# Kernel tuning notes

Hardware: AMD Instinct MI355X
Metric: run time of the kernel (lower is better)

The kernel has to match this reference:

```python
import jax, jax.numpy as jnp
import numpy as np

DIM = 2048
N_HEADS = 32
N_KV_HEADS = 8
HEAD_DIM = DIM // N_HEADS
ROPE_BASE = 10000.0
BATCH = 2
SEQ = 2048


def _rope_cos_sin(seq_len, dtype=jnp.float32):
    inv_freq = 1.0 / (ROPE_BASE ** (jnp.arange(0, HEAD_DIM, 2, dtype=jnp.float32) / HEAD_DIM))
    pos = jnp.arange(seq_len, dtype=jnp.float32)
    freqs = pos[:, None] * inv_freq[None, :]  # (seq, head_dim/2)
    return jnp.cos(freqs).astype(dtype), jnp.sin(freqs).astype(dtype)


def _apply_rope(x, cos, sin):
    # x: (b, h, s, d); cos/sin: (s, d/2). Interleaved (even/odd) RoPE.
    cos = cos[None, None, :, :]
    sin = sin[None, None, :, :]
    x_even = x[..., ::2]
    x_odd = x[..., 1::2]
    rot_even = x_even * cos - x_odd * sin
    rot_odd = x_even * sin + x_odd * cos
    out = jnp.stack((rot_even, rot_odd), axis=-1)
    return out.reshape(x.shape)


def setup_inputs() -> dict:
    key = jax.random.key(0)
    ks = jax.random.split(key, 5)
    s = 0.02
    return {
        "x": jax.random.normal(ks[0], (BATCH, SEQ, DIM), dtype=jnp.float32),
        "wq": jax.random.normal(ks[1], (DIM, N_HEADS * HEAD_DIM), dtype=jnp.float32) * s,
        "wk": jax.random.normal(ks[2], (DIM, N_KV_HEADS * HEAD_DIM), dtype=jnp.float32) * s,
        "wv": jax.random.normal(ks[3], (DIM, N_KV_HEADS * HEAD_DIM), dtype=jnp.float32) * s,
        "wo": jax.random.normal(ks[4], (DIM, DIM), dtype=jnp.float32) * s,
    }


def reference(x, wq, wk, wv, wo):
    b, s, _ = x.shape
    q = (x @ wq).reshape(b, s, N_HEADS, HEAD_DIM).transpose(0, 2, 1, 3)
    k = (x @ wk).reshape(b, s, N_KV_HEADS, HEAD_DIM).transpose(0, 2, 1, 3)
    v = (x @ wv).reshape(b, s, N_KV_HEADS, HEAD_DIM).transpose(0, 2, 1, 3)
    cos, sin = _rope_cos_sin(s, x.dtype)
    q = _apply_rope(q, cos, sin)
    k = _apply_rope(k, cos, sin)
    rep = N_HEADS // N_KV_HEADS
    if rep > 1:
        k = jnp.repeat(k, rep, axis=1)
        v = jnp.repeat(v, rep, axis=1)
    scores = jnp.einsum("bhqd,bhkd->bhqk", q, k) / (HEAD_DIM ** 0.5)
    causal = jnp.tril(jnp.ones((s, s), dtype=bool))
    scores = jnp.where(causal[None, None], scores, -jnp.inf)
    probs = jax.nn.softmax(scores, axis=-1)
    out = jnp.einsum("bhqk,bhkd->bhqd", probs, v)
    out = out.transpose(0, 2, 1, 3).reshape(b, s, DIM)
    return out @ wo
```

## Files before the change

### kernel.cpp

```cpp
#include <hip/hip_runtime.h>
#include <stdint.h>

#define DIM   2048
#define NH    32
#define NKV   8
#define HD    64
#define BATCH 2
#define SEQ   2048

typedef __attribute__((ext_vector_type(8))) short  short8;
typedef __attribute__((ext_vector_type(4))) short  short4v;
typedef __attribute__((ext_vector_type(4))) float  f32x4;

#if __has_builtin(__builtin_amdgcn_exp2f)
#define EXP2(x) __builtin_amdgcn_exp2f(x)
#else
#define EXP2(x) exp2f(x)
#endif

static __device__ __forceinline__ short f2bf(float f) {
  union { float f; uint32_t u; } v; v.f = f;
  uint32_t r = v.u + 0x7FFFu + ((v.u >> 16) & 1u);
  return (short)(r >> 16);
}

static __device__ __forceinline__ uint32_t cvtpk_bf16(float lo, float hi) {
  uint32_t r;
  asm("v_cvt_pk_bf16_f32 %0, %1, %2" : "=v"(r) : "v"(lo), "v"(hi));
  return r;
}

#define GLD16(gp, lp) __builtin_amdgcn_global_load_lds(                      \
    (__attribute__((address_space(1))) void*)(void*)(gp),                    \
    (__attribute__((address_space(3))) void*)(lp), 16, 0, 0)

#define QSCALE 0.1803368801111244f

__global__ void __launch_bounds__(256)
prep_kernel(const float* __restrict__ x, const float* __restrict__ wq,
            const float* __restrict__ wk, const float* __restrict__ wv,
            short* __restrict__ x_bf, short* __restrict__ wq_t,
            short* __restrict__ wk_t, short* __restrict__ wv_t,
            float* __restrict__ ct, float* __restrict__ st) {
  __shared__ float t[32][33];
  int blk = blockIdx.x;
  const int tid = threadIdx.x;
  if (blk < 8192) {
    int i = blk * 256 + tid;
    f32x4 v = *reinterpret_cast<const f32x4*>(x + (size_t)i * 4);
    short4v o;
    o.x = f2bf(v.x); o.y = f2bf(v.y); o.z = f2bf(v.z); o.w = f2bf(v.w);
    *reinterpret_cast<short4v*>(x_bf + (size_t)i * 4) = o;
    return;
  }
  blk -= 8192;
  if (blk < 6144) {
    const float* in; short* out; int C, bx, by;
    if (blk < 4096)      { in = wq; out = wq_t; C = 2048; bx = blk & 63; by = blk >> 6; }
    else if (blk < 5120) { int lo = blk - 4096; in = wk; out = wk_t; C = 512; bx = lo & 15; by = lo >> 4; }
    else                 { int lo = blk - 5120; in = wv; out = wv_t; C = 512; bx = lo & 15; by = lo >> 4; }
    const int c0 = bx * 32, r0 = by * 32;
    const int tx = tid & 31, ty = tid >> 5;
#pragma unroll
    for (int j = 0; j < 32; j += 8)
      t[ty + j][tx] = in[(size_t)(r0 + ty + j) * C + c0 + tx];
    __syncthreads();
#pragma unroll
    for (int j = 0; j < 32; j += 8)
      out[(size_t)(c0 + ty + j) * DIM + r0 + tx] = f2bf(t[tx][ty + j]);
    return;
  }
  blk -= 6144;
  {
    int i = blk * 256 + tid;
    int pos = i >> 5, f = i & 31;
    float inv = powf(10000.0f, -(float)f / 32.0f);
    float th = (float)pos * inv;
    ct[i] = cosf(th);
    st[i] = sinf(th);
  }
}

__global__ void transpose_bf_kernel(const float* __restrict__ in, short* __restrict__ out,
                                    int R, int C) {
  __shared__ float t[32][33];
  int c0 = blockIdx.x * 32, r0 = blockIdx.y * 32;
  int tx = threadIdx.x, ty = threadIdx.y;
#pragma unroll
  for (int j = 0; j < 32; j += 8)
    t[ty + j][tx] = in[(size_t)(r0 + ty + j) * C + c0 + tx];
  __syncthreads();
#pragma unroll
  for (int j = 0; j < 32; j += 8)
    out[(size_t)(c0 + ty + j) * R + r0 + tx] = f2bf(t[tx][ty + j]);
}


__device__ __forceinline__ void mfma_tile(const short* __restrict__ as_,
                                          const short* __restrict__ bs_,
                                          int wr, int wc, int lg, int lr,
                                          f32x4 (&acc)[4][4]) {
  short8 af[4], bq[4];
#pragma unroll
  for (int mt = 0; mt < 4; ++mt) {
    int row = wr * 64 + mt * 16 + lr;
    af[mt] = *(const short8*)&as_[row * 32 + ((lg ^ ((row >> 1) & 3)) << 3)];
  }
#pragma unroll
  for (int nt = 0; nt < 4; ++nt) {
    int row = wc * 64 + nt * 16 + lr;
    bq[nt] = *(const short8*)&bs_[row * 32 + ((lg ^ ((row >> 1) & 3)) << 3)];
  }
  __builtin_amdgcn_s_setprio(1);
#pragma unroll
  for (int mt = 0; mt < 4; ++mt)
#pragma unroll
    for (int nt = 0; nt < 4; ++nt)
      acc[mt][nt] = __builtin_amdgcn_mfma_f32_16x16x32_bf16(af[mt], bq[nt], acc[mt][nt], 0, 0, 0);
  __builtin_amdgcn_s_setprio(0);
}

#define STAGE4(SA, SB) do {                                                  \
    GLD16(pA0, (SA) + w * 512);  GLD16(pA1, (SA) + 2048 + w * 512);          \
    GLD16(pB0, (SB) + w * 512);  GLD16(pB1, (SB) + 2048 + w * 512);          \
    pA0 += 32; pA1 += 32; pB0 += 32; pB1 += 32; } while (0)

#define TILE(CA, CB, SA, SB, DOSTAGE, VM) do {                               \
    asm volatile("s_waitcnt vmcnt(" VM ")" ::: "memory");                    \
    __builtin_amdgcn_s_barrier();                                            \
    __builtin_amdgcn_sched_barrier(0);                                       \
    if (DOSTAGE) { STAGE4(SA, SB); }                                         \
    mfma_tile(CA, CB, wr, wc, lg, lr, acc);                                  \
  } while (0)

__device__ __forceinline__ void gemm_mainloop(const short* __restrict__ A,
                                              const short* __restrict__ Bt,
                                              int m0, int n0,
                                              short* As, short* Bs,
                                              f32x4 (&acc)[4][4]) {
  const int tid = threadIdx.x;
  const int w = tid >> 6, l = tid & 63;
  const int lg = l >> 4, lr = l & 15;
  const int wr = w >> 1, wc = w & 1;
  const int c1 = tid + 256;
  const int r0 = tid >> 2, k0 = ((tid & 3) ^ ((r0 >> 1) & 3)) << 3;
  const int r1 = c1 >> 2,  k1 = ((c1 & 3) ^ ((r1 >> 1) & 3)) << 3;
  const short* pA0 = A + (size_t)(m0 + r0) * DIM + k0;
  const short* pA1 = A + (size_t)(m0 + r1) * DIM + k1;
  const short* pB0 = Bt + (size_t)(n0 + r0) * DIM + k0;
  const short* pB1 = Bt + (size_t)(n0 + r1) * DIM + k1;
  short* A0 = As;            short* B0 = Bs;
  short* A1 = As + 4096;     short* B1 = Bs + 4096;
  short* A2 = As + 8192;     short* B2 = Bs + 8192;

  STAGE4(A0, B0);
  STAGE4(A1, B1);

  for (int it = 0; it < 20; ++it) {
    TILE(A0, B0, A2, B2, true, "4");
    TILE(A1, B1, A0, B0, true, "4");
    TILE(A2, B2, A1, B1, true, "4");
  }
  TILE(A0, B0, A2, B2, true,  "4");
  TILE(A1, B1, A0, B0, true,  "4");
  TILE(A2, B2, A0, B0, false, "4");
  TILE(A0, B0, A1, B1, false, "0");
}

__device__ __forceinline__ int2 xcd_swizzle(int nwg) {
  int id = blockIdx.y * gridDim.x + blockIdx.x;
  int swz = (id & 7) * (nwg >> 3) + (id >> 3);
  return make_int2(swz % gridDim.x, swz / gridDim.x);
}

__global__ void __launch_bounds__(256, 3)
gemm_qkv_kernel(const short* __restrict__ A,
                const short* __restrict__ wqt, const short* __restrict__ wkt,
                const short* __restrict__ wvt,
                short* __restrict__ q_ws, short* __restrict__ k_ws, short* __restrict__ v_ws,
                const float* __restrict__ ct, const float* __restrict__ st) {
  __shared__ __align__(16) short As[12288];
  __shared__ __align__(16) short Bs[12288];
  int2 bxy = xcd_swizzle(24 * 32);
  const int n0g = bxy.x * 128;
  const int m0 = bxy.y * 128;
  int mode, n0;
  const short* Bt;
  short* outp;
  if (n0g < 2048)      { mode = 1; Bt = wqt; n0 = n0g;        outp = q_ws; }
  else if (n0g < 2560) { mode = 2; Bt = wkt; n0 = n0g - 2048; outp = k_ws; }
  else                 { mode = 3; Bt = wvt; n0 = n0g - 2560; outp = v_ws; }

  f32x4 acc[4][4] = {};
  gemm_mainloop(A, Bt, m0, n0, As, Bs, acc);

  const int tid = threadIdx.x;
  const int w = tid >> 6, l = tid & 63;
  const int lg = l >> 4, lr = l & 15;
  const int wr = w >> 1, wc = w & 1;
  const int mrow0 = m0 + wr * 64;
  const int ncol0 = n0 + wc * 64;
#pragma unroll
  for (int mt = 0; mt < 4; ++mt)
#pragma unroll
    for (int nt = 0; nt < 4; ++nt)
#pragma unroll
      for (int i = 0; i < 4; ++i) {
        int m = mrow0 + mt * 16 + lg * 4 + i;
        int n = ncol0 + nt * 16 + lr;
        float v = acc[mt][nt][i];
        int b = m >> 11, s = m & (SEQ - 1);
        int h = n >> 6, d = n & 63;
        if (mode == 3) {
          outp[((size_t)(b * NKV + h) * HD + d) * SEQ + s] = f2bf(v);
        } else {
          float p = __shfl_xor(v, 1);
          float cs = ct[(s << 5) + (d >> 1)];
          float sn = st[(s << 5) + (d >> 1)];
          float r = ((d & 1) == 0) ? (v * cs - p * sn) : (p * sn + v * cs);
          if (mode == 1) {
            r *= QSCALE;
            outp[((size_t)(b * NH + h) * SEQ + s) * HD + d] = f2bf(r);
          } else {
            outp[((size_t)(b * NKV + h) * SEQ + s) * HD + d] = f2bf(r);
          }
        }
      }
}

__global__ void __launch_bounds__(256, 3)
gemm_o_kernel(const short* __restrict__ A, const short* __restrict__ Bt,
              float* __restrict__ out) {
  __shared__ __align__(16) short As[12288];
  __shared__ __align__(16) short Bs[12288];
  int2 bxy = xcd_swizzle(16 * 32);
  const int m0 = bxy.y * 128, n0 = bxy.x * 128;
  f32x4 acc[4][4] = {};
  gemm_mainloop(A, Bt, m0, n0, As, Bs, acc);
  const int tid = threadIdx.x;
  const int w = tid >> 6, l = tid & 63;
  const int lg = l >> 4, lr = l & 15;
  const int wr = w >> 1, wc = w & 1;
#pragma unroll
  for (int mt = 0; mt < 4; ++mt)
#pragma unroll
    for (int nt = 0; nt < 4; ++nt)
#pragma unroll
      for (int i = 0; i < 4; ++i) {
        int m = m0 + wr * 64 + mt * 16 + lg * 4 + i;
        int n = n0 + wc * 64 + nt * 16 + lr;
        out[(size_t)m * DIM + n] = acc[mt][nt][i];
      }
}

__global__ void __launch_bounds__(256, 3)
attn_fwd_kernel(const short* __restrict__ Q, const short* __restrict__ K,
                const short* __restrict__ V, short* __restrict__ O) {
  __shared__ __align__(16) short Ks[3][4096];
  __shared__ __align__(16) short Vs[3][4096];
  const int tid = threadIdx.x;
  const int w = tid >> 6, l = tid & 63;
  const int lg = l >> 4, lr = l & 15;
  const int h = blockIdx.y;
  const int b = blockIdx.z;
  const int kvh = h >> 2;
  const int lh = lg >> 1, sub = (lg & 1) << 2;

  const short* kbase = K + (size_t)(b * NKV + kvh) * SEQ * HD;
  const short* vbase = V + (size_t)(b * NKV + kvh) * HD * SEQ;

  const int c1 = tid + 256;
  const int r0 = tid >> 3, e0 = ((tid & 7) ^ (r0 & 7)) << 3;
  const int r1 = c1 >> 3, e1 = ((c1 & 7) ^ (r1 & 7)) << 3;

  short8 ones;
#pragma unroll
  for (int i = 0; i < 8; ++i) ones[i] = (short)0x3F80;

#define ASTAGE(kvt, KB, VB) do { const int kv_ = (kvt) * 64;                  \
    GLD16(kbase + (size_t)(kv_ + r0) * HD + e0, (KB) + w * 512);              \
    GLD16(kbase + (size_t)(kv_ + r1) * HD + e1, (KB) + 2048 + w * 512);       \
    GLD16(vbase + (size_t)r0 * SEQ + kv_ + e0, (VB) + w * 512);               \
    GLD16(vbase + (size_t)r1 * SEQ + kv_ + e1, (VB) + 2048 + w * 512); } while (0)

  for (int qi = 0; qi < 2; ++qi) {
    const int qblk = (qi == 0) ? (int)blockIdx.x : (31 - (int)blockIdx.x);
    const int q0 = qblk * 64;
    const int qrow = q0 + w * 16 + lr;

    const short* qptr = Q + ((size_t)(b * NH + h) * SEQ + qrow) * HD;
    short8 qf0 = *(const short8*)(qptr + (lg << 3));
    short8 qf1 = *(const short8*)(qptr + 32 + (lg << 3));

    float m_run = 0.f;
    f32x4 oacc[4] = {};
    f32x4 lacc = {};

    short* kb0 = Ks[0]; short* kb1 = Ks[1]; short* kb2 = Ks[2];
    short* vb0 = Vs[0]; short* vb1 = Vs[1]; short* vb2 = Vs[2];

    ASTAGE(0, kb0, vb0);
    if (qblk >= 1) ASTAGE(1, kb1, vb1);

    for (int t = 0; t <= qblk; ++t) {
      if (t < qblk) asm volatile("s_waitcnt vmcnt(4)" ::: "memory");
      else          asm volatile("s_waitcnt vmcnt(0)" ::: "memory");
      __builtin_amdgcn_s_barrier();
      __builtin_amdgcn_sched_barrier(0);
      if (t + 2 <= qblk) ASTAGE(t + 2, kb2, vb2);

      const short* ks = kb0;
      const short* vs = vb0;
      const int kv0 = t * 64;

      short8 ka[4][2];
#pragma unroll
      for (int t4 = 0; t4 < 4; ++t4) {
        int row = t4 * 16 + lr, rx = row & 7;
        ka[t4][0] = *(const short8*)&ks[row * 64 + ((lg ^ rx) << 3)];
        ka[t4][1] = *(const short8*)&ks[row * 64 + (((4 + lg) ^ rx) << 3)];
      }
      short8 vbf[4][2];
#pragma unroll
      for (int nt = 0; nt < 4; ++nt) {
        int row = nt * 16 + lr, rx = row & 7;
#pragma unroll
        for (int ks_ = 0; ks_ < 2; ++ks_) {
          union { short8 s8; short4v hh[2]; } u;
          u.hh[0] = *(const short4v*)&vs[row * 64 + (((4 * ks_ + lh) ^ rx) << 3) + sub];
          u.hh[1] = *(const short4v*)&vs[row * 64 + (((4 * ks_ + 2 + lh) ^ rx) << 3) + sub];
          vbf[nt][ks_] = u.s8;
        }
      }

      f32x4 sacc[4];
      {
        f32x4 seed;
        seed[0] = -m_run; seed[1] = -m_run; seed[2] = -m_run; seed[3] = -m_run;
        __builtin_amdgcn_s_setprio(1);
#pragma unroll
        for (int t4 = 0; t4 < 4; ++t4) {
          f32x4 z = __builtin_amdgcn_mfma_f32_16x16x32_bf16(ka[t4][0], qf0, seed, 0, 0, 0);
          sacc[t4] = __builtin_amdgcn_mfma_f32_16x16x32_bf16(ka[t4][1], qf1, z, 0, 0, 0);
        }
        __builtin_amdgcn_s_setprio(0);
      }

      if (t == qblk) {
#pragma unroll
        for (int t4 = 0; t4 < 4; ++t4)
#pragma unroll
          for (int i = 0; i < 4; ++i)
            if (kv0 + t4 * 16 + lg * 4 + i > qrow) sacc[t4][i] = -__builtin_inff();
      }

      float a0 = fmaxf(fmaxf(sacc[0][0], sacc[0][1]), sacc[0][2]);
      float a1 = fmaxf(fmaxf(sacc[0][3], sacc[1][0]), sacc[1][1]);
      float a2 = fmaxf(fmaxf(sacc[1][2], sacc[1][3]), sacc[2][0]);
      float a3 = fmaxf(fmaxf(sacc[2][1], sacc[2][2]), sacc[2][3]);
      float a4 = fmaxf(fmaxf(sacc[3][0], sacc[3][1]), sacc[3][2]);
      float tm = fmaxf(fmaxf(fmaxf(a0, a1), a2), fmaxf(fmaxf(a3, a4), sacc[3][3]));
      tm = fmaxf(tm, __shfl_xor(tm, 16));
      tm = fmaxf(tm, __shfl_xor(tm, 32));

      if (!__all(tm <= 12.0f)) {
        float d = fmaxf(tm, 0.f);
        float alpha = EXP2(-d);
        float av0 = __shfl(alpha, (lg << 2));
        float av1 = __shfl(alpha, (lg << 2) | 1);
        float av2 = __shfl(alpha, (lg << 2) | 2);
        float av3 = __shfl(alpha, (lg << 2) | 3);
#pragma unroll
        for (int nt = 0; nt < 4; ++nt) {
          oacc[nt][0] *= av0; oacc[nt][1] *= av1;
          oacc[nt][2] *= av2; oacc[nt][3] *= av3;
        }
        lacc[0] *= av0; lacc[1] *= av1; lacc[2] *= av2; lacc[3] *= av3;
        m_run += d;
#pragma unroll
        for (int t4 = 0; t4 < 4; ++t4)
#pragma unroll
          for (int i = 0; i < 4; ++i) sacc[t4][i] -= d;
      }

      union { short8 s8; uint32_t u[4]; } pa0, pa1;
      pa0.u[0] = cvtpk_bf16(EXP2(sacc[0][0]), EXP2(sacc[0][1]));
      pa0.u[1] = cvtpk_bf16(EXP2(sacc[0][2]), EXP2(sacc[0][3]));
      pa0.u[2] = cvtpk_bf16(EXP2(sacc[1][0]), EXP2(sacc[1][1]));
      pa0.u[3] = cvtpk_bf16(EXP2(sacc[1][2]), EXP2(sacc[1][3]));
      pa1.u[0] = cvtpk_bf16(EXP2(sacc[2][0]), EXP2(sacc[2][1]));
      pa1.u[1] = cvtpk_bf16(EXP2(sacc[2][2]), EXP2(sacc[2][3]));
      pa1.u[2] = cvtpk_bf16(EXP2(sacc[3][0]), EXP2(sacc[3][1]));
      pa1.u[3] = cvtpk_bf16(EXP2(sacc[3][2]), EXP2(sacc[3][3]));

      __builtin_amdgcn_s_setprio(1);
#pragma unroll
      for (int nt = 0; nt < 4; ++nt) {
        oacc[nt] = __builtin_amdgcn_mfma_f32_16x16x32_bf16(pa0.s8, vbf[nt][0], oacc[nt], 0, 0, 0);
        oacc[nt] = __builtin_amdgcn_mfma_f32_16x16x32_bf16(pa1.s8, vbf[nt][1], oacc[nt], 0, 0, 0);
      }
      lacc = __builtin_amdgcn_mfma_f32_16x16x32_bf16(pa0.s8, ones, lacc, 0, 0, 0);
      lacc = __builtin_amdgcn_mfma_f32_16x16x32_bf16(pa1.s8, ones, lacc, 0, 0, 0);
      __builtin_amdgcn_s_setprio(0);

      short* tk = kb0; kb0 = kb1; kb1 = kb2; kb2 = tk;
      short* tv = vb0; vb0 = vb1; vb1 = vb2; vb2 = tv;
    }

    float linv0 = 1.f / lacc[0], linv1 = 1.f / lacc[1];
    float linv2 = 1.f / lacc[2], linv3 = 1.f / lacc[3];
#pragma unroll
    for (int nt = 0; nt < 4; ++nt) {
      int d = nt * 16 + lr;
      int qb = q0 + w * 16 + lg * 4;
      O[(size_t)(b * SEQ + qb + 0) * DIM + h * HD + d] = f2bf(oacc[nt][0] * linv0);
      O[(size_t)(b * SEQ + qb + 1) * DIM + h * HD + d] = f2bf(oacc[nt][1] * linv1);
      O[(size_t)(b * SEQ + qb + 2) * DIM + h * HD + d] = f2bf(oacc[nt][2] * linv2);
      O[(size_t)(b * SEQ + qb + 3) * DIM + h * HD + d] = f2bf(oacc[nt][3] * linv3);
    }
    __syncthreads();
  }
#undef ASTAGE
}


extern "C" void kernel_launch(void* const* d_in, const int* in_sizes, int n_in,
                              void* d_out, int out_size, void* d_ws, size_t ws_size,
                              hipStream_t stream) {
  const float* x  = (const float*)d_in[0];
  const float* wq = (const float*)d_in[1];
  const float* wk = (const float*)d_in[2];
  const float* wv = (const float*)d_in[3];
  const float* wo = (const float*)d_in[4];
  float* out = (float*)d_out;
  char* ws = (char*)d_ws;

  short* x_bf  = (short*)(ws + 0);
  short* attn  = (short*)(ws + 0);
  short* q_ws  = (short*)(ws + 16777216);
  short* k_ws  = (short*)(ws + 33554432);
  short* v_ws  = (short*)(ws + 37748736);
  short* wq_t  = (short*)(ws + 41943040);
  short* wo_t  = (short*)(ws + 41943040);
  short* wk_t  = (short*)(ws + 50331648);
  short* wv_t  = (short*)(ws + 52428800);
  float* ct    = (float*)(ws + 54525952);
  float* st    = (float*)(ws + 54788096);
  (void)ws_size; (void)in_sizes; (void)n_in; (void)out_size;

  prep_kernel<<<14592, 256, 0, stream>>>(x, wq, wk, wv, x_bf, wq_t, wk_t, wv_t, ct, st);

  gemm_qkv_kernel<<<dim3(24, 32), 256, 0, stream>>>(x_bf, wq_t, wk_t, wv_t,
                                                    q_ws, k_ws, v_ws, ct, st);

  transpose_bf_kernel<<<dim3(64, 64), dim3(32, 8), 0, stream>>>(wo, wo_t, DIM, 2048);

  attn_fwd_kernel<<<dim3(16, 32, 2), 256, 0, stream>>>(q_ws, k_ws, v_ws, attn);

  gemm_o_kernel<<<dim3(16, 32), 256, 0, stream>>>(attn, wo_t, out);
}
```

Before: 215.0 us.

## Switch GEMMs to 32x32x16 MFMA and fold wo transpose into prep kernel

Replaces the 16x16x32 bf16 MFMA tiles in both projection GEMMs with 32x32x16 MFMA tiles. This needs fewer LDS fragment loads per tile, and the epilogues are remapped to the new accumulator layout. When the workspace is large enough, the wo transpose and bf16 conversion move into the prep kernel with a separate buffer, which removes one kernel launch. Larger accumulator vectors may raise register pressure, and the epilogue store pattern changes.

```diff
diff --git a/kernel.cpp b/kernel.cpp
--- a/kernel.cpp
+++ b/kernel.cpp
@@ -11,6 +11,7 @@
 typedef __attribute__((ext_vector_type(8))) short  short8;
 typedef __attribute__((ext_vector_type(4))) short  short4v;
 typedef __attribute__((ext_vector_type(4))) float  f32x4;
+typedef __attribute__((ext_vector_type(16))) float f32x16;
 
 #if __has_builtin(__builtin_amdgcn_exp2f)
 #define EXP2(x) __builtin_amdgcn_exp2f(x)
@@ -39,8 +40,10 @@
 __global__ void __launch_bounds__(256)
 prep_kernel(const float* __restrict__ x, const float* __restrict__ wq,
             const float* __restrict__ wk, const float* __restrict__ wv,
+            const float* __restrict__ wo,
             short* __restrict__ x_bf, short* __restrict__ wq_t,
             short* __restrict__ wk_t, short* __restrict__ wv_t,
+            short* __restrict__ wo_t,
             float* __restrict__ ct, float* __restrict__ st) {
   __shared__ float t[32][33];
   int blk = blockIdx.x;
@@ -54,11 +57,12 @@
     return;
   }
   blk -= 8192;
-  if (blk < 6144) {
+  if (blk < 6144 || blk >= 6400) {
     const float* in; short* out; int C, bx, by;
     if (blk < 4096)      { in = wq; out = wq_t; C = 2048; bx = blk & 63; by = blk >> 6; }
     else if (blk < 5120) { int lo = blk - 4096; in = wk; out = wk_t; C = 512; bx = lo & 15; by = lo >> 4; }
-    else                 { int lo = blk - 5120; in = wv; out = wv_t; C = 512; bx = lo & 15; by = lo >> 4; }
+    else if (blk < 6144) { int lo = blk - 5120; in = wv; out = wv_t; C = 512; bx = lo & 15; by = lo >> 4; }
+    else                 { int lo = blk - 6400; in = wo; out = wo_t; C = 2048; bx = lo & 63; by = lo >> 6; }
     const int c0 = bx * 32, r0 = by * 32;
     const int tx = tid & 31, ty = tid >> 5;
 #pragma unroll
@@ -70,9 +74,8 @@
       out[(size_t)(c0 + ty + j) * DIM + r0 + tx] = f2bf(t[tx][ty + j]);
     return;
   }
-  blk -= 6144;
   {
-    int i = blk * 256 + tid;
+    int i = (blk - 6144) * 256 + tid;
     int pos = i >> 5, f = i & 31;
     float inv = powf(10000.0f, -(float)f / 32.0f);
     float th = (float)pos * inv;
@@ -96,27 +99,37 @@
 }
 
 
-__device__ __forceinline__ void mfma_tile(const short* __restrict__ as_,
-                                          const short* __restrict__ bs_,
-                                          int wr, int wc, int lg, int lr,
-                                          f32x4 (&acc)[4][4]) {
-  short8 af[4], bq[4];
-#pragma unroll
-  for (int mt = 0; mt < 4; ++mt) {
-    int row = wr * 64 + mt * 16 + lr;
-    af[mt] = *(const short8*)&as_[row * 32 + ((lg ^ ((row >> 1) & 3)) << 3)];
-  }
-#pragma unroll
-  for (int nt = 0; nt < 4; ++nt) {
-    int row = wc * 64 + nt * 16 + lr;
-    bq[nt] = *(const short8*)&bs_[row * 32 + ((lg ^ ((row >> 1) & 3)) << 3)];
+__device__ __forceinline__ void mfma_tile32(const short* __restrict__ as_,
+                                            const short* __restrict__ bs_,
+                                            int wr, int wc, int l,
+                                            f32x16 (&acc)[2][2]) {
+  const int lh = l >> 5, lq = l & 31;
+  short8 af[2][2], bq[2][2];
+#pragma unroll
+  for (int mt = 0; mt < 2; ++mt) {
+    int row = wr * 64 + mt * 32 + lq;
+    int sw = (row >> 1) & 3;
+#pragma unroll
+    for (int ks = 0; ks < 2; ++ks)
+      af[mt][ks] = *(const short8*)&as_[row * 32 + (((ks * 2 + lh) ^ sw) << 3)];
+  }
+#pragma unroll
+  for (int nt = 0; nt < 2; ++nt) {
+    int row = wc * 64 + nt * 32 + lq;
+    int sw = (row >> 1) & 3;
+#pragma unroll
+    for (int ks = 0; ks < 2; ++ks)
+      bq[nt][ks] = *(const short8*)&bs_[row * 32 + (((ks * 2 + lh) ^ sw) << 3)];
   }
   __builtin_amdgcn_s_setprio(1);
 #pragma unroll
-  for (int mt = 0; mt < 4; ++mt)
-#pragma unroll
-    for (int nt = 0; nt < 4; ++nt)
-      acc[mt][nt] = __builtin_amdgcn_mfma_f32_16x16x32_bf16(af[mt], bq[nt], acc[mt][nt], 0, 0, 0);
+  for (int mt = 0; mt < 2; ++mt)
+#pragma unroll
+    for (int nt = 0; nt < 2; ++nt)
+#pragma unroll
+      for (int ks = 0; ks < 2; ++ks)
+        acc[mt][nt] = __builtin_amdgcn_mfma_f32_32x32x16_bf16(af[mt][ks], bq[nt][ks],
+                                                              acc[mt][nt], 0, 0, 0);
   __builtin_amdgcn_s_setprio(0);
 }
 
@@ -130,17 +143,16 @@
     __builtin_amdgcn_s_barrier();                                            \
     __builtin_amdgcn_sched_barrier(0);                                       \
     if (DOSTAGE) { STAGE4(SA, SB); }                                         \
-    mfma_tile(CA, CB, wr, wc, lg, lr, acc);                                  \
+    mfma_tile32(CA, CB, wr, wc, l, acc);                                     \
   } while (0)
 
 __device__ __forceinline__ void gemm_mainloop(const short* __restrict__ A,
                                               const short* __restrict__ Bt,
                                               int m0, int n0,
                                               short* As, short* Bs,
-                                              f32x4 (&acc)[4][4]) {
+                                              f32x16 (&acc)[2][2]) {
   const int tid = threadIdx.x;
   const int w = tid >> 6, l = tid & 63;
-  const int lg = l >> 4, lr = l & 15;
   const int wr = w >> 1, wc = w & 1;
   const int c1 = tid + 256;
   const int r0 = tid >> 2, k0 = ((tid & 3) ^ ((r0 >> 1) & 3)) << 3;
@@ -191,24 +203,24 @@
   else if (n0g < 2560) { mode = 2; Bt = wkt; n0 = n0g - 2048; outp = k_ws; }
   else                 { mode = 3; Bt = wvt; n0 = n0g - 2560; outp = v_ws; }
 
-  f32x4 acc[4][4] = {};
+  f32x16 acc[2][2] = {};
   gemm_mainloop(A, Bt, m0, n0, As, Bs, acc);
 
   const int tid = threadIdx.x;
   const int w = tid >> 6, l = tid & 63;
-  const int lg = l >> 4, lr = l & 15;
   const int wr = w >> 1, wc = w & 1;
-  const int mrow0 = m0 + wr * 64;
-  const int ncol0 = n0 + wc * 64;
-#pragma unroll
-  for (int mt = 0; mt < 4; ++mt)
-#pragma unroll
-    for (int nt = 0; nt < 4; ++nt)
-#pragma unroll
-      for (int i = 0; i < 4; ++i) {
-        int m = mrow0 + mt * 16 + lg * 4 + i;
-        int n = ncol0 + nt * 16 + lr;
-        float v = acc[mt][nt][i];
+  const int lh = l >> 5, lq = l & 31;
+  const int mrow0 = m0 + wr * 64 + lh * 4;
+  const int ncol0 = n0 + wc * 64 + lq;
+#pragma unroll
+  for (int mt = 0; mt < 2; ++mt)
+#pragma unroll
+    for (int nt = 0; nt < 2; ++nt)
+#pragma unroll
+      for (int r = 0; r < 16; ++r) {
+        int m = mrow0 + mt * 32 + (r & 3) + ((r >> 2) << 3);
+        int n = ncol0 + nt * 32;
+        float v = acc[mt][nt][r];
         int b = m >> 11, s = m & (SEQ - 1);
         int h = n >> 6, d = n & 63;
         if (mode == 3) {
@@ -217,12 +229,12 @@
           float p = __shfl_xor(v, 1);
           float cs = ct[(s << 5) + (d >> 1)];
           float sn = st[(s << 5) + (d >> 1)];
-          float r = ((d & 1) == 0) ? (v * cs - p * sn) : (p * sn + v * cs);
+          float rr = ((d & 1) == 0) ? (v * cs - p * sn) : (p * sn + v * cs);
           if (mode == 1) {
-            r *= QSCALE;
-            outp[((size_t)(b * NH + h) * SEQ + s) * HD + d] = f2bf(r);
+            rr *= QSCALE;
+            outp[((size_t)(b * NH + h) * SEQ + s) * HD + d] = f2bf(rr);
           } else {
-            outp[((size_t)(b * NKV + h) * SEQ + s) * HD + d] = f2bf(r);
+            outp[((size_t)(b * NKV + h) * SEQ + s) * HD + d] = f2bf(rr);
           }
         }
       }
@@ -235,21 +247,23 @@
   __shared__ __align__(16) short Bs[12288];
   int2 bxy = xcd_swizzle(16 * 32);
   const int m0 = bxy.y * 128, n0 = bxy.x * 128;
-  f32x4 acc[4][4] = {};
+  f32x16 acc[2][2] = {};
   gemm_mainloop(A, Bt, m0, n0, As, Bs, acc);
   const int tid = threadIdx.x;
   const int w = tid >> 6, l = tid & 63;
-  const int lg = l >> 4, lr = l & 15;
   const int wr = w >> 1, wc = w & 1;
-#pragma unroll
-  for (int mt = 0; mt < 4; ++mt)
-#pragma unroll
-    for (int nt = 0; nt < 4; ++nt)
-#pragma unroll
-      for (int i = 0; i < 4; ++i) {
-        int m = m0 + wr * 64 + mt * 16 + lg * 4 + i;
-        int n = n0 + wc * 64 + nt * 16 + lr;
-        out[(size_t)m * DIM + n] = acc[mt][nt][i];
+  const int lh = l >> 5, lq = l & 31;
+  const int mrow0 = m0 + wr * 64 + lh * 4;
+  const int ncol0 = n0 + wc * 64 + lq;
+#pragma unroll
+  for (int mt = 0; mt < 2; ++mt)
+#pragma unroll
+    for (int nt = 0; nt < 2; ++nt)
+#pragma unroll
+      for (int r = 0; r < 16; ++r) {
+        int m = mrow0 + mt * 32 + (r & 3) + ((r >> 2) << 3);
+        int n = ncol0 + nt * 32;
+        out[(size_t)m * DIM + n] = acc[mt][nt][r];
       }
 }
 
@@ -441,19 +455,22 @@
   short* k_ws  = (short*)(ws + 33554432);
   short* v_ws  = (short*)(ws + 37748736);
   short* wq_t  = (short*)(ws + 41943040);
-  short* wo_t  = (short*)(ws + 41943040);
   short* wk_t  = (short*)(ws + 50331648);
   short* wv_t  = (short*)(ws + 52428800);
   float* ct    = (float*)(ws + 54525952);
   float* st    = (float*)(ws + 54788096);
-  (void)ws_size; (void)in_sizes; (void)n_in; (void)out_size;
-
-  prep_kernel<<<14592, 256, 0, stream>>>(x, wq, wk, wv, x_bf, wq_t, wk_t, wv_t, ct, st);
+  const int sep_wo = (ws_size >= (size_t)63438848);
+  short* wo_t  = sep_wo ? (short*)(ws + 55050240) : wq_t;
+  (void)in_sizes; (void)n_in; (void)out_size;
+
+  prep_kernel<<<sep_wo ? 18688 : 14592, 256, 0, stream>>>(
+      x, wq, wk, wv, wo, x_bf, wq_t, wk_t, wv_t, wo_t, ct, st);
 
   gemm_qkv_kernel<<<dim3(24, 32), 256, 0, stream>>>(x_bf, wq_t, wk_t, wv_t,
                                                     q_ws, k_ws, v_ws, ct, st);
 
-  transpose_bf_kernel<<<dim3(64, 64), dim3(32, 8), 0, stream>>>(wo, wo_t, DIM, 2048);
+  if (!sep_wo)
+    transpose_bf_kernel<<<dim3(64, 64), dim3(32, 8), 0, stream>>>(wo, wo_t, DIM, 2048);
 
   attn_fwd_kernel<<<dim3(16, 32, 2), 256, 0, stream>>>(q_ws, k_ws, v_ws, attn);
 
```

Result: slower. 221.1 us (+2.9%).

## Fold wo transpose into prep kernel and halve attention grid with persistent units

Applied to the files above, without the earlier changes.

When the workspace is large enough, the wo transpose to bf16 is merged into the prep kernel and written to a separate buffer, so one kernel launch goes away. The attention kernel now launches 512 blocks, each handling two (batch, head, q-pair) units in sequence instead of one per block. The aim is to cut launch overhead and the tail from many small blocks, at the cost of fewer blocks in flight and longer serial work per block.

```diff
diff --git a/kernel.cpp b/kernel.cpp
--- a/kernel.cpp
+++ b/kernel.cpp
@@ -39,8 +39,10 @@
 __global__ void __launch_bounds__(256)
 prep_kernel(const float* __restrict__ x, const float* __restrict__ wq,
             const float* __restrict__ wk, const float* __restrict__ wv,
+            const float* __restrict__ wo,
             short* __restrict__ x_bf, short* __restrict__ wq_t,
             short* __restrict__ wk_t, short* __restrict__ wv_t,
+            short* __restrict__ wo_t,
             float* __restrict__ ct, float* __restrict__ st) {
   __shared__ float t[32][33];
   int blk = blockIdx.x;
@@ -54,11 +56,12 @@
     return;
   }
   blk -= 8192;
-  if (blk < 6144) {
+  if (blk < 6144 || blk >= 6400) {
     const float* in; short* out; int C, bx, by;
     if (blk < 4096)      { in = wq; out = wq_t; C = 2048; bx = blk & 63; by = blk >> 6; }
     else if (blk < 5120) { int lo = blk - 4096; in = wk; out = wk_t; C = 512; bx = lo & 15; by = lo >> 4; }
-    else                 { int lo = blk - 5120; in = wv; out = wv_t; C = 512; bx = lo & 15; by = lo >> 4; }
+    else if (blk < 6144) { int lo = blk - 5120; in = wv; out = wv_t; C = 512; bx = lo & 15; by = lo >> 4; }
+    else                 { int lo = blk - 6400; in = wo; out = wo_t; C = 2048; bx = lo & 63; by = lo >> 6; }
     const int c0 = bx * 32, r0 = by * 32;
     const int tx = tid & 31, ty = tid >> 5;
 #pragma unroll
@@ -70,9 +73,8 @@
       out[(size_t)(c0 + ty + j) * DIM + r0 + tx] = f2bf(t[tx][ty + j]);
     return;
   }
-  blk -= 6144;
   {
-    int i = blk * 256 + tid;
+    int i = (blk - 6144) * 256 + tid;
     int pos = i >> 5, f = i & 31;
     float inv = powf(10000.0f, -(float)f / 32.0f);
     float th = (float)pos * inv;
@@ -261,13 +263,7 @@
   const int tid = threadIdx.x;
   const int w = tid >> 6, l = tid & 63;
   const int lg = l >> 4, lr = l & 15;
-  const int h = blockIdx.y;
-  const int b = blockIdx.z;
-  const int kvh = h >> 2;
   const int lh = lg >> 1, sub = (lg & 1) << 2;
-
-  const short* kbase = K + (size_t)(b * NKV + kvh) * SEQ * HD;
-  const short* vbase = V + (size_t)(b * NKV + kvh) * HD * SEQ;
 
   const int c1 = tid + 256;
   const int r0 = tid >> 3, e0 = ((tid & 7) ^ (r0 & 7)) << 3;
@@ -283,142 +279,152 @@
     GLD16(vbase + (size_t)r0 * SEQ + kv_ + e0, (VB) + w * 512);               \
     GLD16(vbase + (size_t)r1 * SEQ + kv_ + e1, (VB) + 2048 + w * 512); } while (0)
 
-  for (int qi = 0; qi < 2; ++qi) {
-    const int qblk = (qi == 0) ? (int)blockIdx.x : (31 - (int)blockIdx.x);
-    const int q0 = qblk * 64;
-    const int qrow = q0 + w * 16 + lr;
-
-    const short* qptr = Q + ((size_t)(b * NH + h) * SEQ + qrow) * HD;
-    short8 qf0 = *(const short8*)(qptr + (lg << 3));
-    short8 qf1 = *(const short8*)(qptr + 32 + (lg << 3));
-
-    float m_run = 0.f;
-    f32x4 oacc[4] = {};
-    f32x4 lacc = {};
-
-    short* kb0 = Ks[0]; short* kb1 = Ks[1]; short* kb2 = Ks[2];
-    short* vb0 = Vs[0]; short* vb1 = Vs[1]; short* vb2 = Vs[2];
-
-    ASTAGE(0, kb0, vb0);
-    if (qblk >= 1) ASTAGE(1, kb1, vb1);
-
-    for (int t = 0; t <= qblk; ++t) {
-      if (t < qblk) asm volatile("s_waitcnt vmcnt(4)" ::: "memory");
-      else          asm volatile("s_waitcnt vmcnt(0)" ::: "memory");
-      __builtin_amdgcn_s_barrier();
-      __builtin_amdgcn_sched_barrier(0);
-      if (t + 2 <= qblk) ASTAGE(t + 2, kb2, vb2);
-
-      const short* ks = kb0;
-      const short* vs = vb0;
-      const int kv0 = t * 64;
-
-      short8 ka[4][2];
-#pragma unroll
-      for (int t4 = 0; t4 < 4; ++t4) {
-        int row = t4 * 16 + lr, rx = row & 7;
-        ka[t4][0] = *(const short8*)&ks[row * 64 + ((lg ^ rx) << 3)];
-        ka[t4][1] = *(const short8*)&ks[row * 64 + (((4 + lg) ^ rx) << 3)];
+  for (int ui = 0; ui < 2; ++ui) {
+    const int u = (int)blockIdx.x + ui * 512;
+    const int b = u >> 9;
+    const int h = (u & 511) >> 4;
+    const int qpair = u & 15;
+    const int kvh = h >> 2;
+    const short* kbase = K + (size_t)(b * NKV + kvh) * SEQ * HD;
+    const short* vbase = V + (size_t)(b * NKV + kvh) * HD * SEQ;
+
+    for (int qi = 0; qi < 2; ++qi) {
+      const int qblk = (qi == 0) ? qpair : (31 - qpair);
+      const int q0 = qblk * 64;
+      const int qrow = q0 + w * 16 + lr;
+
+      const short* qptr = Q + ((size_t)(b * NH + h) * SEQ + qrow) * HD;
+      short8 qf0 = *(const short8*)(qptr + (lg << 3));
+      short8 qf1 = *(const short8*)(qptr + 32 + (lg << 3));
+
+      float m_run = 0.f;
+      f32x4 oacc[4] = {};
+      f32x4 lacc = {};
+
+      short* kb0 = Ks[0]; short* kb1 = Ks[1]; short* kb2 = Ks[2];
+      short* vb0 = Vs[0]; short* vb1 = Vs[1]; short* vb2 = Vs[2];
+
+      ASTAGE(0, kb0, vb0);
+      if (qblk >= 1) ASTAGE(1, kb1, vb1);
+
+      for (int t = 0; t <= qblk; ++t) {
+        if (t < qblk) asm volatile("s_waitcnt vmcnt(4)" ::: "memory");
+        else          asm volatile("s_waitcnt vmcnt(0)" ::: "memory");
+        __builtin_amdgcn_s_barrier();
+        __builtin_amdgcn_sched_barrier(0);
+        if (t + 2 <= qblk) ASTAGE(t + 2, kb2, vb2);
+
+        const short* ks = kb0;
+        const short* vs = vb0;
+        const int kv0 = t * 64;
+
+        short8 ka[4][2];
+#pragma unroll
+        for (int t4 = 0; t4 < 4; ++t4) {
+          int row = t4 * 16 + lr, rx = row & 7;
+          ka[t4][0] = *(const short8*)&ks[row * 64 + ((lg ^ rx) << 3)];
+          ka[t4][1] = *(const short8*)&ks[row * 64 + (((4 + lg) ^ rx) << 3)];
+        }
+        short8 vbf[4][2];
+#pragma unroll
+        for (int nt = 0; nt < 4; ++nt) {
+          int row = nt * 16 + lr, rx = row & 7;
+#pragma unroll
+          for (int ks_ = 0; ks_ < 2; ++ks_) {
+            union { short8 s8; short4v hh[2]; } uu;
+            uu.hh[0] = *(const short4v*)&vs[row * 64 + (((4 * ks_ + lh) ^ rx) << 3) + sub];
+            uu.hh[1] = *(const short4v*)&vs[row * 64 + (((4 * ks_ + 2 + lh) ^ rx) << 3) + sub];
+            vbf[nt][ks_] = uu.s8;
+          }
+        }
+
+        f32x4 sacc[4];
+        {
+          f32x4 seed;
+          seed[0] = -m_run; seed[1] = -m_run; seed[2] = -m_run; seed[3] = -m_run;
+          __builtin_amdgcn_s_setprio(1);
+#pragma unroll
+          for (int t4 = 0; t4 < 4; ++t4) {
+            f32x4 z = __builtin_amdgcn_mfma_f32_16x16x32_bf16(ka[t4][0], qf0, seed, 0, 0, 0);
+            sacc[t4] = __builtin_amdgcn_mfma_f32_16x16x32_bf16(ka[t4][1], qf1, z, 0, 0, 0);
+          }
+          __builtin_amdgcn_s_setprio(0);
+        }
+
+        if (t == qblk) {
+#pragma unroll
+          for (int t4 = 0; t4 < 4; ++t4)
+#pragma unroll
+            for (int i = 0; i < 4; ++i)
+              if (kv0 + t4 * 16 + lg * 4 + i > qrow) sacc[t4][i] = -__builtin_inff();
+        }
+
+        float a0 = fmaxf(fmaxf(sacc[0][0], sacc[0][1]), sacc[0][2]);
+        float a1 = fmaxf(fmaxf(sacc[0][3], sacc[1][0]), sacc[1][1]);
+        float a2 = fmaxf(fmaxf(sacc[1][2], sacc[1][3]), sacc[2][0]);
+        float a3 = fmaxf(fmaxf(sacc[2][1], sacc[2][2]), sacc[2][3]);
+        float a4 = fmaxf(fmaxf(sacc[3][0], sacc[3][1]), sacc[3][2]);
+        float tm = fmaxf(fmaxf(fmaxf(a0, a1), a2), fmaxf(fmaxf(a3, a4), sacc[3][3]));
+        tm = fmaxf(tm, __shfl_xor(tm, 16));
+        tm = fmaxf(tm, __shfl_xor(tm, 32));
+
+        if (!__all(tm <= 12.0f)) {
+          float d = fmaxf(tm, 0.f);
+          float alpha = EXP2(-d);
+          float av0 = __shfl(alpha, (lg << 2));
+          float av1 = __shfl(alpha, (lg << 2) | 1);
+          float av2 = __shfl(alpha, (lg << 2) | 2);
+          float av3 = __shfl(alpha, (lg << 2) | 3);
+#pragma unroll
+          for (int nt = 0; nt < 4; ++nt) {
+            oacc[nt][0] *= av0; oacc[nt][1] *= av1;
+            oacc[nt][2] *= av2; oacc[nt][3] *= av3;
+          }
+          lacc[0] *= av0; lacc[1] *= av1; lacc[2] *= av2; lacc[3] *= av3;
+          m_run += d;
+#pragma unroll
+          for (int t4 = 0; t4 < 4; ++t4)
+#pragma unroll
+            for (int i = 0; i < 4; ++i) sacc[t4][i] -= d;
+        }
+
+        union { short8 s8; uint32_t u[4]; } pa0, pa1;
+        pa0.u[0] = cvtpk_bf16(EXP2(sacc[0][0]), EXP2(sacc[0][1]));
+        pa0.u[1] = cvtpk_bf16(EXP2(sacc[0][2]), EXP2(sacc[0][3]));
+        pa0.u[2] = cvtpk_bf16(EXP2(sacc[1][0]), EXP2(sacc[1][1]));
+        pa0.u[3] = cvtpk_bf16(EXP2(sacc[1][2]), EXP2(sacc[1][3]));
+        pa1.u[0] = cvtpk_bf16(EXP2(sacc[2][0]), EXP2(sacc[2][1]));
+        pa1.u[1] = cvtpk_bf16(EXP2(sacc[2][2]), EXP2(sacc[2][3]));
+        pa1.u[2] = cvtpk_bf16(EXP2(sacc[3][0]), EXP2(sacc[3][1]));
+        pa1.u[3] = cvtpk_bf16(EXP2(sacc[3][2]), EXP2(sacc[3][3]));
+
+        __builtin_amdgcn_s_setprio(1);
+#pragma unroll
+        for (int nt = 0; nt < 4; ++nt) {
+          oacc[nt] = __builtin_amdgcn_mfma_f32_16x16x32_bf16(pa0.s8, vbf[nt][0], oacc[nt], 0, 0, 0);
+          oacc[nt] = __builtin_amdgcn_mfma_f32_16x16x32_bf16(pa1.s8, vbf[nt][1], oacc[nt], 0, 0, 0);
+        }
+        lacc = __builtin_amdgcn_mfma_f32_16x16x32_bf16(pa0.s8, ones, lacc, 0, 0, 0);
+        lacc = __builtin_amdgcn_mfma_f32_16x16x32_bf16(pa1.s8, ones, lacc, 0, 0, 0);
+        __builtin_amdgcn_s_setprio(0);
+
+        short* tk = kb0; kb0 = kb1; kb1 = kb2; kb2 = tk;
+        short* tv = vb0; vb0 = vb1; vb1 = vb2; vb2 = tv;
       }
-      short8 vbf[4][2];
+
+      float linv0 = 1.f / lacc[0], linv1 = 1.f / lacc[1];
+      float linv2 = 1.f / lacc[2], linv3 = 1.f / lacc[3];
 #pragma unroll
       for (int nt = 0; nt < 4; ++nt) {
-        int row = nt * 16 + lr, rx = row & 7;
-#pragma unroll
-        for (int ks_ = 0; ks_ < 2; ++ks_) {
-          union { short8 s8; short4v hh[2]; } u;
-          u.hh[0] = *(const short4v*)&vs[row * 64 + (((4 * ks_ + lh) ^ rx) << 3) + sub];
-          u.hh[1] = *(const short4v*)&vs[row * 64 + (((4 * ks_ + 2 + lh) ^ rx) << 3) + sub];
-          vbf[nt][ks_] = u.s8;
-        }
+        int d = nt * 16 + lr;
+        int qb = q0 + w * 16 + lg * 4;
+        O[(size_t)(b * SEQ + qb + 0) * DIM + h * HD + d] = f2bf(oacc[nt][0] * linv0);
+        O[(size_t)(b * SEQ + qb + 1) * DIM + h * HD + d] = f2bf(oacc[nt][1] * linv1);
+        O[(size_t)(b * SEQ + qb + 2) * DIM + h * HD + d] = f2bf(oacc[nt][2] * linv2);
+        O[(size_t)(b * SEQ + qb + 3) * DIM + h * HD + d] = f2bf(oacc[nt][3] * linv3);
       }
-
-      f32x4 sacc[4];
-      {
-        f32x4 seed;
-        seed[0] = -m_run; seed[1] = -m_run; seed[2] = -m_run; seed[3] = -m_run;
-        __builtin_amdgcn_s_setprio(1);
-#pragma unroll
-        for (int t4 = 0; t4 < 4; ++t4) {
-          f32x4 z = __builtin_amdgcn_mfma_f32_16x16x32_bf16(ka[t4][0], qf0, seed, 0, 0, 0);
-          sacc[t4] = __builtin_amdgcn_mfma_f32_16x16x32_bf16(ka[t4][1], qf1, z, 0, 0, 0);
-        }
-        __builtin_amdgcn_s_setprio(0);
-      }
-
-      if (t == qblk) {
-#pragma unroll
-        for (int t4 = 0; t4 < 4; ++t4)
-#pragma unroll
-          for (int i = 0; i < 4; ++i)
-            if (kv0 + t4 * 16 + lg * 4 + i > qrow) sacc[t4][i] = -__builtin_inff();
-      }
-
-      float a0 = fmaxf(fmaxf(sacc[0][0], sacc[0][1]), sacc[0][2]);
-      float a1 = fmaxf(fmaxf(sacc[0][3], sacc[1][0]), sacc[1][1]);
-      float a2 = fmaxf(fmaxf(sacc[1][2], sacc[1][3]), sacc[2][0]);
-      float a3 = fmaxf(fmaxf(sacc[2][1], sacc[2][2]), sacc[2][3]);
-      float a4 = fmaxf(fmaxf(sacc[3][0], sacc[3][1]), sacc[3][2]);
-      float tm = fmaxf(fmaxf(fmaxf(a0, a1), a2), fmaxf(fmaxf(a3, a4), sacc[3][3]));
-      tm = fmaxf(tm, __shfl_xor(tm, 16));
-      tm = fmaxf(tm, __shfl_xor(tm, 32));
-
-      if (!__all(tm <= 12.0f)) {
-        float d = fmaxf(tm, 0.f);
-        float alpha = EXP2(-d);
-        float av0 = __shfl(alpha, (lg << 2));
-        float av1 = __shfl(alpha, (lg << 2) | 1);
-        float av2 = __shfl(alpha, (lg << 2) | 2);
-        float av3 = __shfl(alpha, (lg << 2) | 3);
-#pragma unroll
-        for (int nt = 0; nt < 4; ++nt) {
-          oacc[nt][0] *= av0; oacc[nt][1] *= av1;
-          oacc[nt][2] *= av2; oacc[nt][3] *= av3;
-        }
-        lacc[0] *= av0; lacc[1] *= av1; lacc[2] *= av2; lacc[3] *= av3;
-        m_run += d;
-#pragma unroll
-        for (int t4 = 0; t4 < 4; ++t4)
-#pragma unroll
-          for (int i = 0; i < 4; ++i) sacc[t4][i] -= d;
-      }
-
-      union { short8 s8; uint32_t u[4]; } pa0, pa1;
-      pa0.u[0] = cvtpk_bf16(EXP2(sacc[0][0]), EXP2(sacc[0][1]));
-      pa0.u[1] = cvtpk_bf16(EXP2(sacc[0][2]), EXP2(sacc[0][3]));
-      pa0.u[2] = cvtpk_bf16(EXP2(sacc[1][0]), EXP2(sacc[1][1]));
-      pa0.u[3] = cvtpk_bf16(EXP2(sacc[1][2]), EXP2(sacc[1][3]));
-      pa1.u[0] = cvtpk_bf16(EXP2(sacc[2][0]), EXP2(sacc[2][1]));
-      pa1.u[1] = cvtpk_bf16(EXP2(sacc[2][2]), EXP2(sacc[2][3]));
-      pa1.u[2] = cvtpk_bf16(EXP2(sacc[3][0]), EXP2(sacc[3][1]));
-      pa1.u[3] = cvtpk_bf16(EXP2(sacc[3][2]), EXP2(sacc[3][3]));
-
-      __builtin_amdgcn_s_setprio(1);
-#pragma unroll
-      for (int nt = 0; nt < 4; ++nt) {
-        oacc[nt] = __builtin_amdgcn_mfma_f32_16x16x32_bf16(pa0.s8, vbf[nt][0], oacc[nt], 0, 0, 0);
-        oacc[nt] = __builtin_amdgcn_mfma_f32_16x16x32_bf16(pa1.s8, vbf[nt][1], oacc[nt], 0, 0, 0);
-      }
-      lacc = __builtin_amdgcn_mfma_f32_16x16x32_bf16(pa0.s8, ones, lacc, 0, 0, 0);
-      lacc = __builtin_amdgcn_mfma_f32_16x16x32_bf16(pa1.s8, ones, lacc, 0, 0, 0);
-      __builtin_amdgcn_s_setprio(0);
-
-      short* tk = kb0; kb0 = kb1; kb1 = kb2; kb2 = tk;
-      short* tv = vb0; vb0 = vb1; vb1 = vb2; vb2 = tv;
+      __syncthreads();
     }
-
-    float linv0 = 1.f / lacc[0], linv1 = 1.f / lacc[1];
-    float linv2 = 1.f / lacc[2], linv3 = 1.f / lacc[3];
-#pragma unroll
-    for (int nt = 0; nt < 4; ++nt) {
-      int d = nt * 16 + lr;
-      int qb = q0 + w * 16 + lg * 4;
-      O[(size_t)(b * SEQ + qb + 0) * DIM + h * HD + d] = f2bf(oacc[nt][0] * linv0);
-      O[(size_t)(b * SEQ + qb + 1) * DIM + h * HD + d] = f2bf(oacc[nt][1] * linv1);
-      O[(size_t)(b * SEQ + qb + 2) * DIM + h * HD + d] = f2bf(oacc[nt][2] * linv2);
-      O[(size_t)(b * SEQ + qb + 3) * DIM + h * HD + d] = f2bf(oacc[nt][3] * linv3);
-    }
-    __syncthreads();
   }
 #undef ASTAGE
 }
@@ -441,21 +447,24 @@
   short* k_ws  = (short*)(ws + 33554432);
   short* v_ws  = (short*)(ws + 37748736);
   short* wq_t  = (short*)(ws + 41943040);
-  short* wo_t  = (short*)(ws + 41943040);
   short* wk_t  = (short*)(ws + 50331648);
   short* wv_t  = (short*)(ws + 52428800);
   float* ct    = (float*)(ws + 54525952);
   float* st    = (float*)(ws + 54788096);
-  (void)ws_size; (void)in_sizes; (void)n_in; (void)out_size;
-
-  prep_kernel<<<14592, 256, 0, stream>>>(x, wq, wk, wv, x_bf, wq_t, wk_t, wv_t, ct, st);
+  const int sep_wo = (ws_size >= (size_t)63438848);
+  short* wo_t  = sep_wo ? (short*)(ws + 55050240) : wq_t;
+  (void)in_sizes; (void)n_in; (void)out_size;
+
+  prep_kernel<<<sep_wo ? 18688 : 14592, 256, 0, stream>>>(
+      x, wq, wk, wv, wo, x_bf, wq_t, wk_t, wv_t, wo_t, ct, st);
 
   gemm_qkv_kernel<<<dim3(24, 32), 256, 0, stream>>>(x_bf, wq_t, wk_t, wv_t,
                                                     q_ws, k_ws, v_ws, ct, st);
 
-  transpose_bf_kernel<<<dim3(64, 64), dim3(32, 8), 0, stream>>>(wo, wo_t, DIM, 2048);
-
-  attn_fwd_kernel<<<dim3(16, 32, 2), 256, 0, stream>>>(q_ws, k_ws, v_ws, attn);
+  if (!sep_wo)
+    transpose_bf_kernel<<<dim3(64, 64), dim3(32, 8), 0, stream>>>(wo, wo_t, DIM, 2048);
+
+  attn_fwd_kernel<<<512, 256, 0, stream>>>(q_ws, k_ws, v_ws, attn);
 
   gemm_o_kernel<<<dim3(16, 32), 256, 0, stream>>>(attn, wo_t, out);
 }
```

After: 225.8 us. 5.0% more time.
